# Kernel optimization log

Hardware: AMD Instinct MI355X
Metric: run time of the kernel (lower is better)

## Reference

```python
import jax, jax.numpy as jnp
import numpy as np

# DAttentionBaseline config (matches init_kwargs)
NH, HC, G = 8, 32, 4          # n_heads, n_head_channels, n_groups
ORF = 2.0                      # offset_range_factor
KK = 5                         # offset conv kernel (stage_idx=2)


def _conv1x1(x, w, b=None):
    # x: (B,C,H,W), w: (O,C)
    y = jnp.einsum('bchw,oc->bohw', x, w)
    return y if b is None else y + b[None, :, None, None]


def _ref_points(Hk, Wk, dtype):
    # replicates torch.meshgrid(..., indexing='xy') as in the source
    ly = jnp.linspace(0.5, Hk - 0.5, Hk, dtype=dtype)
    lx = jnp.linspace(0.5, Wk - 0.5, Wk, dtype=dtype)
    ry, rx = jnp.meshgrid(ly, lx, indexing='xy')  # shapes (Wk, Hk); Hk==Wk here
    return jnp.stack([ry / Hk * 2 - 1, rx / Wk * 2 - 1], axis=-1)  # (Hk,Wk,2)


def _grid_sample(img, grid):
    # bilinear, align_corners=True, zero padding. img:(N,C,Hi,Wi), grid:(N,Hg,Wg,2) in [-1,1] (x,y)
    N, C, Hi, Wi = img.shape
    gx = (grid[..., 0] + 1.0) * 0.5 * (Wi - 1)
    gy = (grid[..., 1] + 1.0) * 0.5 * (Hi - 1)
    x0 = jnp.floor(gx); y0 = jnp.floor(gy)
    x1 = x0 + 1.0;      y1 = y0 + 1.0
    wx1 = gx - x0; wx0 = 1.0 - wx1
    wy1 = gy - y0; wy0 = 1.0 - wy1
    nidx = jnp.arange(N)[:, None, None]

    def gather(yf, xf):
        valid = (xf >= 0) & (xf <= Wi - 1) & (yf >= 0) & (yf <= Hi - 1)
        xi = jnp.clip(xf, 0, Wi - 1).astype(jnp.int32)
        yi = jnp.clip(yf, 0, Hi - 1).astype(jnp.int32)
        vals = img[nidx, :, yi, xi]  # (N,Hg,Wg,C)
        return vals * valid[..., None].astype(img.dtype)

    out = (gather(y0, x0) * (wy0 * wx0)[..., None]
           + gather(y0, x1) * (wy0 * wx1)[..., None]
           + gather(y1, x0) * (wy1 * wx0)[..., None]
           + gather(y1, x1) * (wy1 * wx1)[..., None])
    return out.transpose(0, 3, 1, 2)  # (N,C,Hg,Wg)


def _forward(x, wq, bq, w_off_dw, b_off_dw, ln_g, ln_b, w_off_pj, wk, bk, wv, bv, wo, bo, rpe_table):
    B, C, H, W = x.shape
    GC = C // G            # group channels
    GH = NH // G           # group heads
    scale = HC ** -0.5

    q = _conv1x1(x, wq, bq)                                   # (B,C,H,W)
    q_off = q.reshape(B * G, GC, H, W)

    # conv_offset: depthwise conv -> LayerNorm over channels -> GELU -> 1x1 conv to 2
    off = jax.lax.conv_general_dilated(
        q_off, w_off_dw, (1, 1), [(KK // 2, KK // 2), (KK // 2, KK // 2)],
        feature_group_count=GC, dimension_numbers=('NCHW', 'OIHW', 'NCHW'))
    off = off + b_off_dw[None, :, None, None]
    mu = off.mean(axis=1, keepdims=True)
    var = off.var(axis=1, keepdims=True)
    off = (off - mu) * jax.lax.rsqrt(var + 1e-5)
    off = off * ln_g[None, :, None, None] + ln_b[None, :, None, None]
    off = jax.nn.gelu(off, approximate=False)
    offset = jnp.einsum('bchw,oc->bohw', off, w_off_pj)       # (B*G,2,Hk,Wk)

    Hk, Wk = offset.shape[2], offset.shape[3]
    ns = Hk * Wk
    rng = jnp.array([1.0 / Hk, 1.0 / Wk], dtype=x.dtype).reshape(1, 2, 1, 1)
    offset = jnp.tanh(offset) * rng * ORF                     # offset_range_factor > 0
    offset = offset.transpose(0, 2, 3, 1)                     # (B*G,Hk,Wk,2)

    ref = _ref_points(Hk, Wk, x.dtype)                        # (Hk,Wk,2)
    pos = offset + ref[None]                                  # (B*G,Hk,Wk,2), (y,x) order

    xs = _grid_sample(x.reshape(B * G, GC, H, W), pos[..., ::-1])  # (B*G,GC,Hk,Wk)
    xs = xs.reshape(B, C, 1, ns)

    k = _conv1x1(xs, wk, bk).reshape(B * NH, HC, ns)
    v = _conv1x1(xs, wv, bv).reshape(B * NH, HC, ns)
    qf = q.reshape(B * NH, HC, H * W)
    attn = jnp.einsum('bcm,bcn->bmn', qf, k) * scale          # (B*NH, HW, ns)

    # RPE via grid_sample on the (2H-1, 2W-1) bias table
    rpe = jnp.broadcast_to(rpe_table[None], (B,) + rpe_table.shape)
    rpe = rpe.reshape(B * G, GH, 2 * H - 1, 2 * W - 1)
    qg = _ref_points(H, W, x.dtype).reshape(H * W, 2)
    disp = (qg[None, :, None, :] - pos.reshape(B * G, ns, 2)[:, None, :, :]) * 0.5  # (B*G,HW,ns,2)
    bias = _grid_sample(rpe, disp[..., ::-1]).reshape(B * NH, H * W, ns)
    attn = attn + bias

    attn = jax.nn.softmax(attn, axis=2)
    out = jnp.einsum('bmn,bcn->bcm', attn, v).reshape(B, C, H, W)
    y = _conv1x1(out, wo, bo)
    return (y,
            pos.reshape(B, G, Hk, Wk, 2),
            jnp.broadcast_to(ref[None, None], (B, G, Hk, Wk, 2)))


def setup_inputs() -> dict:
    key = jax.random.key(0)
    ks = jax.random.split(key, 8)
    B, C, H, W = 4, 256, 32, 32
    GC = C // G
    s = 0.02

    def n(k, shape, sc=s):
        return jax.random.normal(k, shape, jnp.float32) * sc

    return {
        'x': jax.random.normal(ks[0], (B, C, H, W), jnp.float32),
        'wq': n(ks[1], (C, C)), 'bq': jnp.zeros((C,), jnp.float32),
        'w_off_dw': n(ks[2], (GC, 1, KK, KK)), 'b_off_dw': jnp.zeros((GC,), jnp.float32),
        'ln_g': jnp.ones((GC,), jnp.float32), 'ln_b': jnp.zeros((GC,), jnp.float32),
        'w_off_pj': n(ks[3], (2, GC)),
        'wk': n(ks[4], (C, C)), 'bk': jnp.zeros((C,), jnp.float32),
        'wv': n(ks[5], (C, C)), 'bv': jnp.zeros((C,), jnp.float32),
        'wo': n(ks[6], (C, C)), 'bo': jnp.zeros((C,), jnp.float32),
        'rpe_table': n(ks[7], (NH, 2 * H - 1, 2 * W - 1), 0.01),
    }


def reference(x, wq, bq, w_off_dw, b_off_dw, ln_g, ln_b, w_off_pj, wk, bk, wv, bv, wo, bo, rpe_table):
    return _forward(x, wq, bq, w_off_dw, b_off_dw, ln_g, ln_b, w_off_pj, wk, bk, wv, bv, wo, bo, rpe_table)
```

## Files before the change

kernel.cpp:

```cpp
#include <hip/hip_runtime.h>
#include <math.h>

#define CK __restrict__

constexpr int CH = 256;
constexpr int HW = 1024;

typedef __attribute__((ext_vector_type(8))) short short8;
typedef __attribute__((ext_vector_type(4))) float f32x4;

__device__ __forceinline__ ushort f2b(float x) {
    union { float f; unsigned int u; } a; a.f = x;
    unsigned int r = (a.u + 0x7FFFu + ((a.u >> 16) & 1u)) >> 16;
    return (ushort)r;
}
__device__ __forceinline__ short8 ld8(const ushort* p) { return *(const short8*)p; }
__device__ __forceinline__ float u2f(unsigned int u) {
    union { unsigned int u; float f; } a; a.u = u; return a.f;
}
__device__ __forceinline__ float b2f(ushort us) { return u2f((unsigned int)us << 16); }

__global__ __launch_bounds__(256) void prep(const float* CK w0, const float* CK w1,
                                            const float* CK w2, const float* CK w3,
                                            ushort* CK o0, ushort* CK o1,
                                            ushort* CK o2, ushort* CK o3,
                                            const float* CK x, ushort* CK xT,
                                            const float* CK rpe, unsigned int* CK rpetab) {
    const int bid = blockIdx.x, t = threadIdx.x;
    if (bid < 256) {
        const float* src; ushort* dst;
        switch (bid >> 6) {
            case 0: src = w0; dst = o0; break;
            case 1: src = w1; dst = o1; break;
            case 2: src = w2; dst = o2; break;
            default: src = w3; dst = o3; break;
        }
        const int i = (bid & 63) * 256 + t;
        float4 v = ((const float4*)src)[i];
        ushort4 r; r.x = f2b(v.x); r.y = f2b(v.y); r.z = f2b(v.z); r.w = f2b(v.w);
        ((ushort4*)dst)[i] = r;
    } else if (bid < 384) {
        const int b2 = bid - 256;
        const int c8 = b2 & 31, b = b2 >> 5;
        for (int nn = 0; nn < 4; nn++) {
            const int n = nn * 256 + t;
            union { ushort u[8]; short8 s; } pk;
#pragma unroll
            for (int j = 0; j < 8; j++) pk.u[j] = f2b(x[(b * 256 + c8 * 8 + j) * HW + n]);
            *(short8*)(xT + b * 262144 + n * 256 + c8 * 8) = pk.s;
        }
    } else {
        const int h = bid - 384;
        const float* rp = rpe + h * 3969;
        unsigned int* dst = rpetab + h * 4356;
        for (int i = t; i < 4356; i += 256) {
            int y = i / 67, x2 = i - y * 67;
            int yy = y - 1, xx = x2 - 1;
            bool vy = (yy >= 0) && (yy < 63) && (y < 65);
            float a  = (vy && xx >= 0 && xx < 63) ? rp[yy * 63 + xx] : 0.f;
            float bb = (vy && xx >= -1 && xx < 62) ? rp[yy * 63 + xx + 1] : 0.f;
            dst[i] = (unsigned int)f2b(a) | ((unsigned int)f2b(bb) << 16);
        }
    }
}

__global__ __launch_bounds__(256) void gemm_f32(const ushort* CK AT, const ushort* CK W,
                                                const float* CK bias, float* CK Y) {
    const int b = blockIdx.z;
    const int t = threadIdx.x, w = t >> 6, l = t & 63;
    const int lm = l & 15, qd = l >> 4;
    const int m0 = blockIdx.y * 16;
    const int np = blockIdx.x * 64 + w * 16;
    const ushort* A  = AT + b * 262144 + (np + lm) * 256;
    const ushort* Bm = W + (m0 + lm) * 256;
    f32x4 acc = {0.f, 0.f, 0.f, 0.f};
#pragma unroll
    for (int k0 = 0; k0 < 8; k0++) {
        const int ko = k0 * 32 + qd * 8;
        acc = __builtin_amdgcn_mfma_f32_16x16x32_bf16(ld8(A + ko), ld8(Bm + ko), acc, 0, 0, 0);
    }
    const float bs = bias[m0 + lm];
    float4 r;
    r.x = acc[0] + bs; r.y = acc[1] + bs; r.z = acc[2] + bs; r.w = acc[3] + bs;
    *(float4*)(Y + b * 262144 + (m0 + lm) * HW + np + qd * 4) = r;
}

__global__ __launch_bounds__(256) void gemm_kv(const ushort* CK AT,
                                               const ushort* CK Wk, const float* CK bk, ushort* CK kbt,
                                               const ushort* CK Wv, const float* CK bv, ushort* CK vbs) {
    const int b = blockIdx.z;
    const int t = threadIdx.x, w = t >> 6, l = t & 63;
    const int lm = l & 15, qd = l >> 4;
    const int m0 = blockIdx.y * 16;
    const int np = blockIdx.x * 64 + w * 16;
    const ushort* A  = AT + b * 262144 + (np + lm) * 256;
    const ushort* Kw = Wk + (m0 + lm) * 256;
    const ushort* Vw = Wv + (m0 + lm) * 256;
    f32x4 akT = {0.f, 0.f, 0.f, 0.f}, av = {0.f, 0.f, 0.f, 0.f};
#pragma unroll
    for (int k0 = 0; k0 < 8; k0++) {
        const int ko = k0 * 32 + qd * 8;
        short8 a = ld8(A + ko);
        akT = __builtin_amdgcn_mfma_f32_16x16x32_bf16(ld8(Kw + ko), a, akT, 0, 0, 0);
        av  = __builtin_amdgcn_mfma_f32_16x16x32_bf16(a, ld8(Vw + ko), av, 0, 0, 0);
    }
    {
        const int ch0 = m0 + qd * 4;
        const int pix = np + lm;
        const int bh = b * 8 + (ch0 >> 5);
        const int qdk = (ch0 & 31) >> 3, co4 = ch0 & 7;
        const int nc = pix >> 7, nbk = (pix >> 4) & 7, lmk = pix & 15;
        const float4 bks = *(const float4*)(bk + ch0);
        ushort4 r4;
        r4.x = f2b(akT[0] + bks.x); r4.y = f2b(akT[1] + bks.y);
        r4.z = f2b(akT[2] + bks.z); r4.w = f2b(akT[3] + bks.w);
        *(ushort4*)(kbt + ((bh * 8 + nc) * 512 + nbk * 64 + qdk * 16 + lmk) * 8 + co4) = r4;
    }
    {
        const int ch = m0 + lm;
        const int pix0 = np + qd * 4;
        const int bh = b * 8 + (ch >> 5);
        const int cb = (ch & 31) >> 4, lmv = ch & 15;
        const int nc = pix0 >> 7, kc = (pix0 >> 5) & 3;
        const int qdv = (pix0 >> 3) & 3, co0 = pix0 & 7;
        const float bs = bv[ch];
        ushort4 r4;
        r4.x = f2b(av[0] + bs); r4.y = f2b(av[1] + bs);
        r4.z = f2b(av[2] + bs); r4.w = f2b(av[3] + bs);
        *(ushort4*)(vbs + ((bh * 8 + nc) * 512 + (cb * 4 + kc) * 64 + qdv * 16 + lmv) * 8 + co0) = r4;
    }
}

__global__ __launch_bounds__(256) void dwconv(const float* CK q, const float* CK wdw,
                                              const float* CK bdw, float* CK off) {
    const int bx = blockIdx.x;
    const int ch = bx & 63;
    const float* qb = q + bx * HW;
    float w[25];
#pragma unroll
    for (int i = 0; i < 25; i++) w[i] = wdw[ch * 25 + i];
    const float bb = bdw[ch];
    const int t = threadIdx.x;
#pragma unroll
    for (int p = 0; p < 4; p++) {
        int hw = p * 256 + t;
        int ii = hw >> 5, jj = hw & 31;
        float s = bb;
#pragma unroll
        for (int ky = 0; ky < 5; ky++) {
            int y = ii + ky - 2;
            if (y < 0 || y > 31) continue;
#pragma unroll
            for (int kx = 0; kx < 5; kx++) {
                int x = jj + kx - 2;
                if (x < 0 || x > 31) continue;
                s += qb[y * 32 + x] * w[ky * 5 + kx];
            }
        }
        off[bx * HW + hw] = s;
    }
}

__global__ __launch_bounds__(256) void lnps(const float* CK off, const float* CK ln_g,
                                            const float* CK ln_b, const float* CK wpj,
                                            const float* CK x,
                                            float* CK out_pos, float* CK out_ref,
                                            float2* CK pos_sc, ushort* CK xsT) {
    const int bid = blockIdx.x, t = threadIdx.x;
    const int bg = bid >> 4;
    const int pix_l = t >> 2, qtr = t & 3;
    const int n = (bid & 15) * 64 + pix_l;
    const int gid = bg * 1024 + n;
    const float* ob = off + bg * 64 * HW + n;
    const int c0 = qtr * 16;
    float s1 = 0.f;
#pragma unroll
    for (int j = 0; j < 16; j++) s1 += ob[(c0 + j) * HW];
    s1 += __shfl_xor(s1, 1); s1 += __shfl_xor(s1, 2);
    const float mean = s1 * 0.015625f;
    float s2 = 0.f;
#pragma unroll
    for (int j = 0; j < 16; j++) { float d = ob[(c0 + j) * HW] - mean; s2 += d * d; }
    s2 += __shfl_xor(s2, 1); s2 += __shfl_xor(s2, 2);
    const float rs = rsqrtf(s2 * 0.015625f + 1e-5f);
    float p0 = 0.f, p1 = 0.f;
#pragma unroll
    for (int j = 0; j < 16; j++) {
        float vv = (ob[(c0 + j) * HW] - mean) * rs * ln_g[c0 + j] + ln_b[c0 + j];
        float gl = 0.5f * vv * (1.f + erff(vv * 0.70710678118654752f));
        p0 += gl * wpj[c0 + j];
        p1 += gl * wpj[64 + c0 + j];
    }
    p0 += __shfl_xor(p0, 1); p0 += __shfl_xor(p0, 2);
    p1 += __shfl_xor(p1, 1); p1 += __shfl_xor(p1, 2);
    const int ii = n >> 5, jj = n & 31;
    const float r0 = (jj + 0.5f) * 0.0625f - 1.f;
    const float r1 = (ii + 0.5f) * 0.0625f - 1.f;
    const float pos0 = tanhf(p0) * 0.0625f + r0;
    const float pos1 = tanhf(p1) * 0.0625f + r1;
    if (qtr == 0) {
        out_pos[gid * 2] = pos0; out_pos[gid * 2 + 1] = pos1;
        out_ref[gid * 2] = r0;   out_ref[gid * 2 + 1] = r1;
        pos_sc[gid].x = pos0 * 15.5f; pos_sc[gid].y = pos1 * 15.5f;
    }
    const float gx = (pos1 + 1.f) * 15.5f, gy = (pos0 + 1.f) * 15.5f;
    const float x0f = floorf(gx), y0f = floorf(gy);
    const float wx1 = gx - x0f, wx0 = 1.f - wx1, wy1 = gy - y0f, wy0 = 1.f - wy1;
    const bool vx0 = (x0f >= 0.f) && (x0f <= 31.f);
    const bool vx1 = (x0f >= -1.f) && (x0f <= 30.f);
    const bool vy0 = (y0f >= 0.f) && (y0f <= 31.f);
    const bool vy1 = (y0f >= -1.f) && (y0f <= 30.f);
    const int xi0 = (int)fminf(fmaxf(x0f, 0.f), 31.f);
    const int xi1 = (int)fminf(fmaxf(x0f + 1.f, 0.f), 31.f);
    const int yi0 = (int)fminf(fmaxf(y0f, 0.f), 31.f);
    const int yi1 = (int)fminf(fmaxf(y0f + 1.f, 0.f), 31.f);
    const float w00 = (vy0 && vx0) ? wy0 * wx0 : 0.f;
    const float w01 = (vy0 && vx1) ? wy0 * wx1 : 0.f;
    const float w10 = (vy1 && vx0) ? wy1 * wx0 : 0.f;
    const float w11 = (vy1 && vx1) ? wy1 * wx1 : 0.f;
    const int o00 = yi0 * 32 + xi0, o01 = yi0 * 32 + xi1;
    const int o10 = yi1 * 32 + xi0, o11 = yi1 * 32 + xi1;
    const int b = bg >> 2, g = bg & 3;
    const float* xb = x + bg * 64 * HW;
    ushort* xo = xsT + b * 262144 + n * 256 + g * 64 + c0;
#pragma unroll
    for (int j4 = 0; j4 < 4; j4++) {
        ushort4 r4;
        float vals[4];
#pragma unroll
        for (int j = 0; j < 4; j++) {
            const float* p = xb + (c0 + j4 * 4 + j) * HW;
            vals[j] = w00 * p[o00] + w01 * p[o01] + w10 * p[o10] + w11 * p[o11];
        }
        r4.x = f2b(vals[0]); r4.y = f2b(vals[1]); r4.z = f2b(vals[2]); r4.w = f2b(vals[3]);
        *(ushort4*)(xo + j4 * 4) = r4;
    }
}

__global__ __launch_bounds__(256, 4) void attn_part(const float* CK q, const ushort* CK kbt,
                                                    const ushort* CK vbs, const float2* CK pos_sc,
                                                    const unsigned int* CK rpetab,
                                                    ushort* CK partO, float2* CK mlbuf) {
    __shared__ __align__(16) unsigned int rpe_pr[4356];
    __shared__ __align__(16) ushort Pl[4][2176];
    const int bh = blockIdx.y, half = blockIdx.z;
    const int b = bh >> 3, nh = bh & 7, bg = bh >> 1;
    const int t = threadIdx.x;
    const int w = t >> 6, l = t & 63;
    const int lm = l & 15, qd = l >> 4;

    {
        const uint4* src4 = (const uint4*)(rpetab + nh * 4356);
        uint4* dst4 = (uint4*)rpe_pr;
        for (int i = t; i < 1089; i += 256) dst4[i] = src4[i];
    }
    __syncthreads();

    const int m = blockIdx.x * 64 + w * 16 + lm;
    short8 qf;
    {
        union { ushort u[8]; short8 s; } pk;
        const float* qb = q + (b * 256 + nh * 32) * HW + m;
#pragma unroll
        for (int j = 0; j < 8; j++) pk.u[j] = f2b(qb[(qd * 8 + j) * HW]);
        qf = pk.s;
    }
    const float qg0 = ((m & 31) + 0.5f) * 0.0625f - 1.f;
    const float qg1 = ((m >> 5) + 0.5f) * 0.0625f - 1.f;
    const float ax = 31.f + 15.5f * qg1;
    const float ay = 31.f + 15.5f * qg0;

    f32x4 oacc0 = {0.f, 0.f, 0.f, 0.f}, oacc1 = {0.f, 0.f, 0.f, 0.f};
    float rmax = -3e38f, rsum = 0.f;
    ushort* PlW = Pl[w];
    const float2* pbase = pos_sc + bg * 1024;

    for (int nc = half * 4; nc < half * 4 + 4; nc++) {
        const ushort* kg = kbt + (bh * 8 + nc) * 4096;
        const ushort* vg = vbs + (bh * 8 + nc) * 4096;

        f32x4 sT[8];
#pragma unroll
        for (int nb = 0; nb < 8; nb++) {
            sT[nb] = __builtin_amdgcn_mfma_f32_16x16x32_bf16(ld8(kg + (nb * 64 + l) * 8), qf,
                        (f32x4){0.f, 0.f, 0.f, 0.f}, 0, 0, 0);
        }

        float cmax = -3e38f;
#pragma unroll
        for (int nb = 0; nb < 8; nb++) {
            const float4* pp = (const float4*)(pbase + nc * 128 + nb * 16 + qd * 4);
            const float4 pa = pp[0], pb_ = pp[1];
            const float psx[4] = {pa.x, pa.z, pb_.x, pb_.z};
            const float psy[4] = {pa.y, pa.w, pb_.y, pb_.w};
#pragma unroll
            for (int r = 0; r < 4; r++) {
                const float gx = ax - psy[r];
                const float gy = ay - psx[r];
                const float x0f = floorf(gx), y0f = floorf(gy);
                const float wx1 = gx - x0f, wy1 = gy - y0f;
                const int idx = (int)y0f * 67 + (int)x0f + 68;
                const unsigned int pr0 = rpe_pr[idx];
                const unsigned int pr1 = rpe_pr[idx + 67];
                const float t00 = u2f(pr0 << 16), t01 = u2f(pr0 & 0xFFFF0000u);
                const float t10 = u2f(pr1 << 16), t11 = u2f(pr1 & 0xFFFF0000u);
                const float u0 = t00 + wx1 * (t01 - t00);
                const float u1 = t10 + wx1 * (t11 - t10);
                const float bias = u0 + wy1 * (u1 - u0);
                sT[nb][r] = sT[nb][r] * 0.17677669529663687f + bias;
                cmax = fmaxf(cmax, sT[nb][r]);
            }
        }
        cmax = fmaxf(cmax, __shfl_xor(cmax, 16));
        cmax = fmaxf(cmax, __shfl_xor(cmax, 32));
        const float newmax = fmaxf(rmax, cmax);
        const float alpha = __expf(rmax - newmax);
        rmax = newmax;

        float csum = 0.f;
#pragma unroll
        for (int nb = 0; nb < 8; nb++) {
            float e0 = __expf(sT[nb][0] - rmax);
            float e1 = __expf(sT[nb][1] - rmax);
            float e2 = __expf(sT[nb][2] - rmax);
            float e3 = __expf(sT[nb][3] - rmax);
            csum += (e0 + e1) + (e2 + e3);
            uint2 pk;
            pk.x = (unsigned int)f2b(e0) | ((unsigned int)f2b(e1) << 16);
            pk.y = (unsigned int)f2b(e2) | ((unsigned int)f2b(e3) << 16);
            *(uint2*)(PlW + nb * 272 + l * 4) = pk;
        }
        csum += __shfl_xor(csum, 16);
        csum += __shfl_xor(csum, 32);
        rsum = rsum * alpha + csum;
        oacc0 *= alpha;
        oacc1 *= alpha;

#pragma unroll
        for (int kc = 0; kc < 4; kc++) {
            const ushort* pb2 = PlW + (kc * 2 + (qd >> 1)) * 272 + (qd & 1) * 128 + lm * 4;
            union { uint2 u[2]; short8 s; } pfu;
            pfu.u[0] = *(const uint2*)pb2;
            pfu.u[1] = *(const uint2*)(pb2 + 64);
            oacc0 = __builtin_amdgcn_mfma_f32_16x16x32_bf16(ld8(vg + (kc * 64 + l) * 8), pfu.s, oacc0, 0, 0, 0);
            oacc1 = __builtin_amdgcn_mfma_f32_16x16x32_bf16(ld8(vg + ((4 + kc) * 64 + l) * 8), pfu.s, oacc1, 0, 0, 0);
        }
    }

    ushort* po = partO + (((half * 32 + bh) * 1024 + m) * 32) + qd * 4;
    ushort4 r04, r14;
    r04.x = f2b(oacc0[0]); r04.y = f2b(oacc0[1]); r04.z = f2b(oacc0[2]); r04.w = f2b(oacc0[3]);
    r14.x = f2b(oacc1[0]); r14.y = f2b(oacc1[1]); r14.z = f2b(oacc1[2]); r14.w = f2b(oacc1[3]);
    *(ushort4*)po = r04;
    *(ushort4*)(po + 16) = r14;
    if (qd == 0) {
        float2 ml; ml.x = rmax; ml.y = rsum;
        mlbuf[(half * 32 + bh) * 1024 + m] = ml;
    }
}

__global__ __launch_bounds__(256) void attn_comb(const ushort* CK partO, const float2* CK mlbuf,
                                                 ushort* CK aoT) {
    const int gid = blockIdx.x * 256 + threadIdx.x;
    const int bh = gid >> 10, m = gid & 1023;
    const int b = bh >> 3, nh = bh & 7;
    const float2 ml0 = mlbuf[bh * 1024 + m];
    const float2 ml1 = mlbuf[(32 + bh) * 1024 + m];
    const float M = fmaxf(ml0.x, ml1.x);
    const float e0 = __expf(ml0.x - M), e1 = __expf(ml1.x - M);
    const float inv = 1.f / (ml0.y * e0 + ml1.y * e1);
    const float w0 = e0 * inv, w1 = e1 * inv;
    const ushort* p0 = partO + (bh * 1024 + m) * 32;
    const ushort* p1 = partO + ((32 + bh) * 1024 + m) * 32;
    ushort* ob = aoT + b * 262144 + m * 256 + nh * 32;
#pragma unroll
    for (int h = 0; h < 2; h++) {
        union { ushort u[8]; short8 s; } a, c, o;
        a.s = ld8(p0 + h * 8 + (h >> 1) * 0);
        a.s = ld8(p0 + h * 16);
        c.s = ld8(p1 + h * 16);
#pragma unroll
        for (int j = 0; j < 8; j++) o.u[j] = f2b(b2f(a.u[j]) * w0 + b2f(c.u[j]) * w1);
        *(short8*)(ob + h * 16) = o.s;
        union { ushort u[8]; short8 s; } a2, c2, o2;
        a2.s = ld8(p0 + h * 16 + 8);
        c2.s = ld8(p1 + h * 16 + 8);
#pragma unroll
        for (int j = 0; j < 8; j++) o2.u[j] = f2b(b2f(a2.u[j]) * w0 + b2f(c2.u[j]) * w1);
        *(short8*)(ob + h * 16 + 8) = o2.s;
    }
}

extern "C" void kernel_launch(void* const* d_in, const int* in_sizes, int n_in,
                              void* d_out, int out_size, void* d_ws, size_t ws_size,
                              hipStream_t stream) {
    (void)in_sizes; (void)n_in; (void)out_size; (void)ws_size;
    const float* x   = (const float*)d_in[0];
    const float* wq  = (const float*)d_in[1];
    const float* bq  = (const float*)d_in[2];
    const float* wdw = (const float*)d_in[3];
    const float* bdw = (const float*)d_in[4];
    const float* lng = (const float*)d_in[5];
    const float* lnb = (const float*)d_in[6];
    const float* wpj = (const float*)d_in[7];
    const float* wk  = (const float*)d_in[8];
    const float* bk  = (const float*)d_in[9];
    const float* wv  = (const float*)d_in[10];
    const float* bv  = (const float*)d_in[11];
    const float* wo  = (const float*)d_in[12];
    const float* bo  = (const float*)d_in[13];
    const float* rpe = (const float*)d_in[14];
    float* outp = (float*)d_out;
    char* base = (char*)d_ws;
    const size_t MB = 1 << 20;

    float*  q_ws   = (float*)(base);
    float*  off_ws = (float*)(base + 4 * MB);
    ushort* partO  = (ushort*)(base + 4 * MB);
    float2* pos_sc = (float2*)(base + 8 * MB);
    ushort* xT     = (ushort*)(base + 8 * MB + 131072);
    float2* mlbuf  = (float2*)(base + 8 * MB + 131072);
    ushort* xsT    = (ushort*)(base + 10 * MB + 131072);
    ushort* kbt    = (ushort*)(base + 12 * MB + 131072);
    ushort* vbs    = (ushort*)(base + 14 * MB + 131072);
    ushort* aoT    = (ushort*)(base + 16 * MB + 131072);
    ushort* wqb    = (ushort*)(base + 18 * MB + 131072);
    ushort* wkb    = (ushort*)(base + 18 * MB + 262144);
    ushort* wvb    = (ushort*)(base + 18 * MB + 393216);
    ushort* wob    = (ushort*)(base + 18 * MB + 524288);
    unsigned int* rpetab = (unsigned int*)(base + 18 * MB + 655360);

    prep<<<392, 256, 0, stream>>>(wq, wk, wv, wo, wqb, wkb, wvb, wob, x, xT, rpe, rpetab);
    gemm_f32<<<dim3(16, 16, 4), 256, 0, stream>>>(xT, wqb, bq, q_ws);
    dwconv<<<1024, 256, 0, stream>>>(q_ws, wdw, bdw, off_ws);
    lnps<<<256, 256, 0, stream>>>(off_ws, lng, lnb, wpj, x,
                                  outp + (1 << 20), outp + (1 << 20) + 32768, pos_sc, xsT);
    gemm_kv<<<dim3(16, 16, 4), 256, 0, stream>>>(xsT, wkb, bk, kbt, wvb, bv, vbs);
    attn_part<<<dim3(16, 32, 2), 256, 0, stream>>>(q_ws, kbt, vbs, pos_sc, rpetab, partO, mlbuf);
    attn_comb<<<128, 256, 0, stream>>>(partO, mlbuf, aoT);
    gemm_f32<<<dim3(16, 16, 4), 256, 0, stream>>>(aoT, wob, bo, outp);
}
```

Measured before the change: 202.8 us.

## Retile GEMMs to 32x32 per wave, store q in bf16, split attention four ways

The GEMMs now have each wave compute a 2x2 block of 16x16 MFMA tiles, so A and B fragments are reused and the grid is a quarter of its former size. The Q projection output is written as bf16, which halves its traffic into dwconv and attention and removes the conversion inside attention. Attention splits keys into four partitions instead of two, processes keys in smaller chunks with a smaller LDS buffer and a higher occupancy hint, and the combine kernel merges four partials. LayerNorm caches its loaded values in registers, and the workspace layout is reorganised. Rounding q to bf16 earlier slightly changes the numerics of the offset path, and the finer online-softmax chunks add more rescaling steps.

```diff
diff --git a/kernel.cpp b/kernel.cpp
--- a/kernel.cpp
+++ b/kernel.cpp
@@ -64,25 +64,74 @@
     }
 }
 
-__global__ __launch_bounds__(256) void gemm_f32(const ushort* CK AT, const ushort* CK W,
-                                                const float* CK bias, float* CK Y) {
+__global__ __launch_bounds__(256) void gemm_q(const ushort* CK AT, const ushort* CK W,
+                                              const float* CK bias, ushort* CK Y) {
     const int b = blockIdx.z;
     const int t = threadIdx.x, w = t >> 6, l = t & 63;
     const int lm = l & 15, qd = l >> 4;
-    const int m0 = blockIdx.y * 16;
-    const int np = blockIdx.x * 64 + w * 16;
-    const ushort* A  = AT + b * 262144 + (np + lm) * 256;
-    const ushort* Bm = W + (m0 + lm) * 256;
-    f32x4 acc = {0.f, 0.f, 0.f, 0.f};
+    const int m0 = blockIdx.y * 64 + (w & 1) * 32;
+    const int n0 = blockIdx.x * 64 + (w >> 1) * 32;
+    const ushort* A = AT + b * 262144 + n0 * 256;
+    const ushort* Bm = W + m0 * 256;
+    f32x4 acc[2][2] = {};
 #pragma unroll
     for (int k0 = 0; k0 < 8; k0++) {
         const int ko = k0 * 32 + qd * 8;
-        acc = __builtin_amdgcn_mfma_f32_16x16x32_bf16(ld8(A + ko), ld8(Bm + ko), acc, 0, 0, 0);
-    }
-    const float bs = bias[m0 + lm];
-    float4 r;
-    r.x = acc[0] + bs; r.y = acc[1] + bs; r.z = acc[2] + bs; r.w = acc[3] + bs;
-    *(float4*)(Y + b * 262144 + (m0 + lm) * HW + np + qd * 4) = r;
+        short8 a0 = ld8(A + lm * 256 + ko);
+        short8 a1 = ld8(A + (16 + lm) * 256 + ko);
+        short8 b0 = ld8(Bm + lm * 256 + ko);
+        short8 b1 = ld8(Bm + (16 + lm) * 256 + ko);
+        acc[0][0] = __builtin_amdgcn_mfma_f32_16x16x32_bf16(a0, b0, acc[0][0], 0, 0, 0);
+        acc[0][1] = __builtin_amdgcn_mfma_f32_16x16x32_bf16(a0, b1, acc[0][1], 0, 0, 0);
+        acc[1][0] = __builtin_amdgcn_mfma_f32_16x16x32_bf16(a1, b0, acc[1][0], 0, 0, 0);
+        acc[1][1] = __builtin_amdgcn_mfma_f32_16x16x32_bf16(a1, b1, acc[1][1], 0, 0, 0);
+    }
+#pragma unroll
+    for (int in = 0; in < 2; in++)
+#pragma unroll
+        for (int im = 0; im < 2; im++) {
+            const int m = m0 + im * 16 + lm;
+            const float bs = bias[m];
+            ushort4 r;
+            r.x = f2b(acc[in][im][0] + bs); r.y = f2b(acc[in][im][1] + bs);
+            r.z = f2b(acc[in][im][2] + bs); r.w = f2b(acc[in][im][3] + bs);
+            *(ushort4*)(Y + b * 262144 + m * HW + n0 + in * 16 + qd * 4) = r;
+        }
+}
+
+__global__ __launch_bounds__(256) void gemm_o(const ushort* CK AT, const ushort* CK W,
+                                              const float* CK bias, float* CK Y) {
+    const int b = blockIdx.z;
+    const int t = threadIdx.x, w = t >> 6, l = t & 63;
+    const int lm = l & 15, qd = l >> 4;
+    const int m0 = blockIdx.y * 64 + (w & 1) * 32;
+    const int n0 = blockIdx.x * 64 + (w >> 1) * 32;
+    const ushort* A = AT + b * 262144 + n0 * 256;
+    const ushort* Bm = W + m0 * 256;
+    f32x4 acc[2][2] = {};
+#pragma unroll
+    for (int k0 = 0; k0 < 8; k0++) {
+        const int ko = k0 * 32 + qd * 8;
+        short8 a0 = ld8(A + lm * 256 + ko);
+        short8 a1 = ld8(A + (16 + lm) * 256 + ko);
+        short8 b0 = ld8(Bm + lm * 256 + ko);
+        short8 b1 = ld8(Bm + (16 + lm) * 256 + ko);
+        acc[0][0] = __builtin_amdgcn_mfma_f32_16x16x32_bf16(a0, b0, acc[0][0], 0, 0, 0);
+        acc[0][1] = __builtin_amdgcn_mfma_f32_16x16x32_bf16(a0, b1, acc[0][1], 0, 0, 0);
+        acc[1][0] = __builtin_amdgcn_mfma_f32_16x16x32_bf16(a1, b0, acc[1][0], 0, 0, 0);
+        acc[1][1] = __builtin_amdgcn_mfma_f32_16x16x32_bf16(a1, b1, acc[1][1], 0, 0, 0);
+    }
+#pragma unroll
+    for (int in = 0; in < 2; in++)
+#pragma unroll
+        for (int im = 0; im < 2; im++) {
+            const int m = m0 + im * 16 + lm;
+            const float bs = bias[m];
+            float4 r;
+            r.x = acc[in][im][0] + bs; r.y = acc[in][im][1] + bs;
+            r.z = acc[in][im][2] + bs; r.w = acc[in][im][3] + bs;
+            *(float4*)(Y + b * 262144 + m * HW + n0 + in * 16 + qd * 4) = r;
+        }
 }
 
 __global__ __launch_bounds__(256) void gemm_kv(const ushort* CK AT,
@@ -91,51 +140,69 @@
     const int b = blockIdx.z;
     const int t = threadIdx.x, w = t >> 6, l = t & 63;
     const int lm = l & 15, qd = l >> 4;
-    const int m0 = blockIdx.y * 16;
-    const int np = blockIdx.x * 64 + w * 16;
-    const ushort* A  = AT + b * 262144 + (np + lm) * 256;
-    const ushort* Kw = Wk + (m0 + lm) * 256;
-    const ushort* Vw = Wv + (m0 + lm) * 256;
-    f32x4 akT = {0.f, 0.f, 0.f, 0.f}, av = {0.f, 0.f, 0.f, 0.f};
+    const int m0 = blockIdx.y * 64 + (w & 1) * 32;
+    const int n0 = blockIdx.x * 64 + (w >> 1) * 32;
+    const ushort* A = AT + b * 262144 + n0 * 256;
+    const ushort* Bk = Wk + m0 * 256;
+    const ushort* Bv = Wv + m0 * 256;
+    f32x4 akT[2][2] = {}, av[2][2] = {};
 #pragma unroll
     for (int k0 = 0; k0 < 8; k0++) {
         const int ko = k0 * 32 + qd * 8;
-        short8 a = ld8(A + ko);
-        akT = __builtin_amdgcn_mfma_f32_16x16x32_bf16(ld8(Kw + ko), a, akT, 0, 0, 0);
-        av  = __builtin_amdgcn_mfma_f32_16x16x32_bf16(a, ld8(Vw + ko), av, 0, 0, 0);
-    }
-    {
-        const int ch0 = m0 + qd * 4;
-        const int pix = np + lm;
-        const int bh = b * 8 + (ch0 >> 5);
-        const int qdk = (ch0 & 31) >> 3, co4 = ch0 & 7;
-        const int nc = pix >> 7, nbk = (pix >> 4) & 7, lmk = pix & 15;
-        const float4 bks = *(const float4*)(bk + ch0);
-        ushort4 r4;
-        r4.x = f2b(akT[0] + bks.x); r4.y = f2b(akT[1] + bks.y);
-        r4.z = f2b(akT[2] + bks.z); r4.w = f2b(akT[3] + bks.w);
-        *(ushort4*)(kbt + ((bh * 8 + nc) * 512 + nbk * 64 + qdk * 16 + lmk) * 8 + co4) = r4;
-    }
-    {
-        const int ch = m0 + lm;
-        const int pix0 = np + qd * 4;
-        const int bh = b * 8 + (ch >> 5);
-        const int cb = (ch & 31) >> 4, lmv = ch & 15;
-        const int nc = pix0 >> 7, kc = (pix0 >> 5) & 3;
-        const int qdv = (pix0 >> 3) & 3, co0 = pix0 & 7;
-        const float bs = bv[ch];
-        ushort4 r4;
-        r4.x = f2b(av[0] + bs); r4.y = f2b(av[1] + bs);
-        r4.z = f2b(av[2] + bs); r4.w = f2b(av[3] + bs);
-        *(ushort4*)(vbs + ((bh * 8 + nc) * 512 + (cb * 4 + kc) * 64 + qdv * 16 + lmv) * 8 + co0) = r4;
-    }
-}
-
-__global__ __launch_bounds__(256) void dwconv(const float* CK q, const float* CK wdw,
+        short8 a0 = ld8(A + lm * 256 + ko);
+        short8 a1 = ld8(A + (16 + lm) * 256 + ko);
+        short8 k0f = ld8(Bk + lm * 256 + ko);
+        short8 k1f = ld8(Bk + (16 + lm) * 256 + ko);
+        short8 v0f = ld8(Bv + lm * 256 + ko);
+        short8 v1f = ld8(Bv + (16 + lm) * 256 + ko);
+        akT[0][0] = __builtin_amdgcn_mfma_f32_16x16x32_bf16(k0f, a0, akT[0][0], 0, 0, 0);
+        akT[0][1] = __builtin_amdgcn_mfma_f32_16x16x32_bf16(k0f, a1, akT[0][1], 0, 0, 0);
+        akT[1][0] = __builtin_amdgcn_mfma_f32_16x16x32_bf16(k1f, a0, akT[1][0], 0, 0, 0);
+        akT[1][1] = __builtin_amdgcn_mfma_f32_16x16x32_bf16(k1f, a1, akT[1][1], 0, 0, 0);
+        av[0][0] = __builtin_amdgcn_mfma_f32_16x16x32_bf16(a0, v0f, av[0][0], 0, 0, 0);
+        av[0][1] = __builtin_amdgcn_mfma_f32_16x16x32_bf16(a0, v1f, av[0][1], 0, 0, 0);
+        av[1][0] = __builtin_amdgcn_mfma_f32_16x16x32_bf16(a1, v0f, av[1][0], 0, 0, 0);
+        av[1][1] = __builtin_amdgcn_mfma_f32_16x16x32_bf16(a1, v1f, av[1][1], 0, 0, 0);
+    }
+#pragma unroll
+    for (int im = 0; im < 2; im++)
+#pragma unroll
+        for (int in = 0; in < 2; in++) {
+            {
+                const int c0 = m0 + im * 16 + qd * 4;
+                const int n  = n0 + in * 16 + lm;
+                const int bh = b * 8 + (c0 >> 5);
+                const int qdk = (c0 & 31) >> 3, co4 = c0 & 7;
+                const int nc = n >> 7, nbk = (n >> 4) & 7, lmk = n & 15;
+                const float4 bks = *(const float4*)(bk + c0);
+                ushort4 r4;
+                r4.x = f2b(akT[im][in][0] + bks.x);
+                r4.y = f2b(akT[im][in][1] + bks.y);
+                r4.z = f2b(akT[im][in][2] + bks.z);
+                r4.w = f2b(akT[im][in][3] + bks.w);
+                *(ushort4*)(kbt + ((bh * 8 + nc) * 512 + nbk * 64 + qdk * 16 + lmk) * 8 + co4) = r4;
+            }
+            {
+                const int c = m0 + im * 16 + lm;
+                const int bh = b * 8 + (c >> 5);
+                const float bs = bv[c];
+                const int cb = (c & 31) >> 4, lmv = c & 15;
+                const int nbase = n0 + in * 16 + qd * 4;
+                const int nc = nbase >> 7, kc = (nbase >> 5) & 3;
+                const int qdv = (nbase >> 3) & 3, co0 = nbase & 7;
+                ushort4 r4;
+                r4.x = f2b(av[in][im][0] + bs); r4.y = f2b(av[in][im][1] + bs);
+                r4.z = f2b(av[in][im][2] + bs); r4.w = f2b(av[in][im][3] + bs);
+                *(ushort4*)(vbs + ((bh * 8 + nc) * 512 + (cb * 4 + kc) * 64 + qdv * 16 + lmv) * 8 + co0) = r4;
+            }
+        }
+}
+
+__global__ __launch_bounds__(256) void dwconv(const ushort* CK q, const float* CK wdw,
                                               const float* CK bdw, float* CK off) {
     const int bx = blockIdx.x;
     const int ch = bx & 63;
-    const float* qb = q + bx * HW;
+    const ushort* qb = q + bx * HW;
     float w[25];
 #pragma unroll
     for (int i = 0; i < 25; i++) w[i] = wdw[ch * 25 + i];
@@ -154,7 +221,7 @@
             for (int kx = 0; kx < 5; kx++) {
                 int x = jj + kx - 2;
                 if (x < 0 || x > 31) continue;
-                s += qb[y * 32 + x] * w[ky * 5 + kx];
+                s += b2f(qb[y * 32 + x]) * w[ky * 5 + kx];
             }
         }
         off[bx * HW + hw] = s;
@@ -173,20 +240,21 @@
     const int gid = bg * 1024 + n;
     const float* ob = off + bg * 64 * HW + n;
     const int c0 = qtr * 16;
+    float v[16];
     float s1 = 0.f;
 #pragma unroll
-    for (int j = 0; j < 16; j++) s1 += ob[(c0 + j) * HW];
+    for (int j = 0; j < 16; j++) { v[j] = ob[(c0 + j) * HW]; s1 += v[j]; }
     s1 += __shfl_xor(s1, 1); s1 += __shfl_xor(s1, 2);
     const float mean = s1 * 0.015625f;
     float s2 = 0.f;
 #pragma unroll
-    for (int j = 0; j < 16; j++) { float d = ob[(c0 + j) * HW] - mean; s2 += d * d; }
+    for (int j = 0; j < 16; j++) { float d = v[j] - mean; s2 += d * d; }
     s2 += __shfl_xor(s2, 1); s2 += __shfl_xor(s2, 2);
     const float rs = rsqrtf(s2 * 0.015625f + 1e-5f);
     float p0 = 0.f, p1 = 0.f;
 #pragma unroll
     for (int j = 0; j < 16; j++) {
-        float vv = (ob[(c0 + j) * HW] - mean) * rs * ln_g[c0 + j] + ln_b[c0 + j];
+        float vv = (v[j] - mean) * rs * ln_g[c0 + j] + ln_b[c0 + j];
         float gl = 0.5f * vv * (1.f + erff(vv * 0.70710678118654752f));
         p0 += gl * wpj[c0 + j];
         p1 += gl * wpj[64 + c0 + j];
@@ -237,13 +305,13 @@
     }
 }
 
-__global__ __launch_bounds__(256, 4) void attn_part(const float* CK q, const ushort* CK kbt,
+__global__ __launch_bounds__(256, 7) void attn_part(const ushort* CK q, const ushort* CK kbt,
                                                     const ushort* CK vbs, const float2* CK pos_sc,
                                                     const unsigned int* CK rpetab,
                                                     ushort* CK partO, float2* CK mlbuf) {
     __shared__ __align__(16) unsigned int rpe_pr[4356];
-    __shared__ __align__(16) ushort Pl[4][2176];
-    const int bh = blockIdx.y, half = blockIdx.z;
+    __shared__ __align__(16) ushort Pl[4][544];
+    const int bh = blockIdx.y, quarter = blockIdx.z;
     const int b = bh >> 3, nh = bh & 7, bg = bh >> 1;
     const int t = threadIdx.x;
     const int w = t >> 6, l = t & 63;
@@ -260,9 +328,9 @@
     short8 qf;
     {
         union { ushort u[8]; short8 s; } pk;
-        const float* qb = q + (b * 256 + nh * 32) * HW + m;
-#pragma unroll
-        for (int j = 0; j < 8; j++) pk.u[j] = f2b(qb[(qd * 8 + j) * HW]);
+        const ushort* qb = q + (b * 256 + nh * 32) * HW + m;
+#pragma unroll
+        for (int j = 0; j < 8; j++) pk.u[j] = qb[(qd * 8 + j) * HW];
         qf = pk.s;
     }
     const float qg0 = ((m & 31) + 0.5f) * 0.0625f - 1.f;
@@ -275,79 +343,77 @@
     ushort* PlW = Pl[w];
     const float2* pbase = pos_sc + bg * 1024;
 
-    for (int nc = half * 4; nc < half * 4 + 4; nc++) {
+    for (int nc = quarter * 2; nc < quarter * 2 + 2; nc++) {
         const ushort* kg = kbt + (bh * 8 + nc) * 4096;
         const ushort* vg = vbs + (bh * 8 + nc) * 4096;
 
-        f32x4 sT[8];
-#pragma unroll
-        for (int nb = 0; nb < 8; nb++) {
-            sT[nb] = __builtin_amdgcn_mfma_f32_16x16x32_bf16(ld8(kg + (nb * 64 + l) * 8), qf,
-                        (f32x4){0.f, 0.f, 0.f, 0.f}, 0, 0, 0);
-        }
-
-        float cmax = -3e38f;
-#pragma unroll
-        for (int nb = 0; nb < 8; nb++) {
-            const float4* pp = (const float4*)(pbase + nc * 128 + nb * 16 + qd * 4);
-            const float4 pa = pp[0], pb_ = pp[1];
-            const float psx[4] = {pa.x, pa.z, pb_.x, pb_.z};
-            const float psy[4] = {pa.y, pa.w, pb_.y, pb_.w};
-#pragma unroll
-            for (int r = 0; r < 4; r++) {
-                const float gx = ax - psy[r];
-                const float gy = ay - psx[r];
-                const float x0f = floorf(gx), y0f = floorf(gy);
-                const float wx1 = gx - x0f, wy1 = gy - y0f;
-                const int idx = (int)y0f * 67 + (int)x0f + 68;
-                const unsigned int pr0 = rpe_pr[idx];
-                const unsigned int pr1 = rpe_pr[idx + 67];
-                const float t00 = u2f(pr0 << 16), t01 = u2f(pr0 & 0xFFFF0000u);
-                const float t10 = u2f(pr1 << 16), t11 = u2f(pr1 & 0xFFFF0000u);
-                const float u0 = t00 + wx1 * (t01 - t00);
-                const float u1 = t10 + wx1 * (t11 - t10);
-                const float bias = u0 + wy1 * (u1 - u0);
-                sT[nb][r] = sT[nb][r] * 0.17677669529663687f + bias;
-                cmax = fmaxf(cmax, sT[nb][r]);
+#pragma unroll
+        for (int nb2 = 0; nb2 < 4; nb2++) {
+            f32x4 sT[2];
+#pragma unroll
+            for (int s = 0; s < 2; s++) {
+                const int nb = nb2 * 2 + s;
+                sT[s] = __builtin_amdgcn_mfma_f32_16x16x32_bf16(
+                            ld8(kg + (nb * 64 + l) * 8), qf,
+                            (f32x4){0.f, 0.f, 0.f, 0.f}, 0, 0, 0);
             }
-        }
-        cmax = fmaxf(cmax, __shfl_xor(cmax, 16));
-        cmax = fmaxf(cmax, __shfl_xor(cmax, 32));
-        const float newmax = fmaxf(rmax, cmax);
-        const float alpha = __expf(rmax - newmax);
-        rmax = newmax;
-
-        float csum = 0.f;
-#pragma unroll
-        for (int nb = 0; nb < 8; nb++) {
-            float e0 = __expf(sT[nb][0] - rmax);
-            float e1 = __expf(sT[nb][1] - rmax);
-            float e2 = __expf(sT[nb][2] - rmax);
-            float e3 = __expf(sT[nb][3] - rmax);
-            csum += (e0 + e1) + (e2 + e3);
-            uint2 pk;
-            pk.x = (unsigned int)f2b(e0) | ((unsigned int)f2b(e1) << 16);
-            pk.y = (unsigned int)f2b(e2) | ((unsigned int)f2b(e3) << 16);
-            *(uint2*)(PlW + nb * 272 + l * 4) = pk;
-        }
-        csum += __shfl_xor(csum, 16);
-        csum += __shfl_xor(csum, 32);
-        rsum = rsum * alpha + csum;
-        oacc0 *= alpha;
-        oacc1 *= alpha;
-
-#pragma unroll
-        for (int kc = 0; kc < 4; kc++) {
-            const ushort* pb2 = PlW + (kc * 2 + (qd >> 1)) * 272 + (qd & 1) * 128 + lm * 4;
+            float cmax = -3e38f;
+#pragma unroll
+            for (int s = 0; s < 2; s++) {
+                const float4* pp = (const float4*)(pbase + nc * 128 + (nb2 * 2 + s) * 16 + qd * 4);
+                const float4 pa = pp[0], pb_ = pp[1];
+                const float psx[4] = {pa.x, pa.z, pb_.x, pb_.z};
+                const float psy[4] = {pa.y, pa.w, pb_.y, pb_.w};
+#pragma unroll
+                for (int r = 0; r < 4; r++) {
+                    const float gx = ax - psy[r];
+                    const float gy = ay - psx[r];
+                    const float x0f = floorf(gx), y0f = floorf(gy);
+                    const float wx1 = gx - x0f, wy1 = gy - y0f;
+                    const int idx = (int)y0f * 67 + (int)x0f + 68;
+                    const unsigned int pr0 = rpe_pr[idx];
+                    const unsigned int pr1 = rpe_pr[idx + 67];
+                    const float t00 = u2f(pr0 << 16), t01 = u2f(pr0 & 0xFFFF0000u);
+                    const float t10 = u2f(pr1 << 16), t11 = u2f(pr1 & 0xFFFF0000u);
+                    const float u0 = t00 + wx1 * (t01 - t00);
+                    const float u1 = t10 + wx1 * (t11 - t10);
+                    sT[s][r] = sT[s][r] * 0.17677669529663687f + (u0 + wy1 * (u1 - u0));
+                    cmax = fmaxf(cmax, sT[s][r]);
+                }
+            }
+            cmax = fmaxf(cmax, __shfl_xor(cmax, 16));
+            cmax = fmaxf(cmax, __shfl_xor(cmax, 32));
+            const float newmax = fmaxf(rmax, cmax);
+            const float alpha = __expf(rmax - newmax);
+            rmax = newmax;
+            float csum = 0.f;
+#pragma unroll
+            for (int s = 0; s < 2; s++) {
+                float e0 = __expf(sT[s][0] - rmax);
+                float e1 = __expf(sT[s][1] - rmax);
+                float e2 = __expf(sT[s][2] - rmax);
+                float e3 = __expf(sT[s][3] - rmax);
+                csum += (e0 + e1) + (e2 + e3);
+                uint2 pk;
+                pk.x = (unsigned int)f2b(e0) | ((unsigned int)f2b(e1) << 16);
+                pk.y = (unsigned int)f2b(e2) | ((unsigned int)f2b(e3) << 16);
+                *(uint2*)(PlW + s * 272 + l * 4) = pk;
+            }
+            csum += __shfl_xor(csum, 16);
+            csum += __shfl_xor(csum, 32);
+            rsum = rsum * alpha + csum;
+            oacc0 *= alpha;
+            oacc1 *= alpha;
+            const ushort* pb2 = PlW + (qd >> 1) * 272 + (qd & 1) * 128 + lm * 4;
             union { uint2 u[2]; short8 s; } pfu;
             pfu.u[0] = *(const uint2*)pb2;
             pfu.u[1] = *(const uint2*)(pb2 + 64);
-            oacc0 = __builtin_amdgcn_mfma_f32_16x16x32_bf16(ld8(vg + (kc * 64 + l) * 8), pfu.s, oacc0, 0, 0, 0);
-            oacc1 = __builtin_amdgcn_mfma_f32_16x16x32_bf16(ld8(vg + ((4 + kc) * 64 + l) * 8), pfu.s, oacc1, 0, 0, 0);
-        }
-    }
-
-    ushort* po = partO + (((half * 32 + bh) * 1024 + m) * 32) + qd * 4;
+            oacc0 = __builtin_amdgcn_mfma_f32_16x16x32_bf16(ld8(vg + (nb2 * 64 + l) * 8), pfu.s, oacc0, 0, 0, 0);
+            oacc1 = __builtin_amdgcn_mfma_f32_16x16x32_bf16(ld8(vg + ((4 + nb2) * 64 + l) * 8), pfu.s, oacc1, 0, 0, 0);
+        }
+    }
+
+    ushort* po = partO + (((quarter * 32 + bh) * 1024 + m) * 32) + qd * 4;
     ushort4 r04, r14;
     r04.x = f2b(oacc0[0]); r04.y = f2b(oacc0[1]); r04.z = f2b(oacc0[2]); r04.w = f2b(oacc0[3]);
     r14.x = f2b(oacc1[0]); r14.y = f2b(oacc1[1]); r14.z = f2b(oacc1[2]); r14.w = f2b(oacc1[3]);
@@ -355,39 +421,40 @@
     *(ushort4*)(po + 16) = r14;
     if (qd == 0) {
         float2 ml; ml.x = rmax; ml.y = rsum;
-        mlbuf[(half * 32 + bh) * 1024 + m] = ml;
-    }
-}
-
-__global__ __launch_bounds__(256) void attn_comb(const ushort* CK partO, const float2* CK mlbuf,
+        mlbuf[(quarter * 32 + bh) * 1024 + m] = ml;
+    }
+}
+
+__global__ __launch_bounds__(128) void attn_comb(const ushort* CK partO, const float2* CK mlbuf,
                                                  ushort* CK aoT) {
-    const int gid = blockIdx.x * 256 + threadIdx.x;
+    const int gid = blockIdx.x * 128 + threadIdx.x;
     const int bh = gid >> 10, m = gid & 1023;
     const int b = bh >> 3, nh = bh & 7;
-    const float2 ml0 = mlbuf[bh * 1024 + m];
-    const float2 ml1 = mlbuf[(32 + bh) * 1024 + m];
-    const float M = fmaxf(ml0.x, ml1.x);
-    const float e0 = __expf(ml0.x - M), e1 = __expf(ml1.x - M);
-    const float inv = 1.f / (ml0.y * e0 + ml1.y * e1);
-    const float w0 = e0 * inv, w1 = e1 * inv;
-    const ushort* p0 = partO + (bh * 1024 + m) * 32;
-    const ushort* p1 = partO + ((32 + bh) * 1024 + m) * 32;
+    float2 ml[4];
+    float M = -3e38f;
+#pragma unroll
+    for (int i = 0; i < 4; i++) { ml[i] = mlbuf[(i * 32 + bh) * 1024 + m]; M = fmaxf(M, ml[i].x); }
+    float e[4], denom = 0.f;
+#pragma unroll
+    for (int i = 0; i < 4; i++) { e[i] = __expf(ml[i].x - M); denom += ml[i].y * e[i]; }
+    const float inv = 1.f / denom;
+#pragma unroll
+    for (int i = 0; i < 4; i++) e[i] *= inv;
     ushort* ob = aoT + b * 262144 + m * 256 + nh * 32;
 #pragma unroll
-    for (int h = 0; h < 2; h++) {
-        union { ushort u[8]; short8 s; } a, c, o;
-        a.s = ld8(p0 + h * 8 + (h >> 1) * 0);
-        a.s = ld8(p0 + h * 16);
-        c.s = ld8(p1 + h * 16);
-#pragma unroll
-        for (int j = 0; j < 8; j++) o.u[j] = f2b(b2f(a.u[j]) * w0 + b2f(c.u[j]) * w1);
-        *(short8*)(ob + h * 16) = o.s;
-        union { ushort u[8]; short8 s; } a2, c2, o2;
-        a2.s = ld8(p0 + h * 16 + 8);
-        c2.s = ld8(p1 + h * 16 + 8);
-#pragma unroll
-        for (int j = 0; j < 8; j++) o2.u[j] = f2b(b2f(a2.u[j]) * w0 + b2f(c2.u[j]) * w1);
-        *(short8*)(ob + h * 16 + 8) = o2.s;
+    for (int g8 = 0; g8 < 4; g8++) {
+        float acc[8] = {};
+#pragma unroll
+        for (int i = 0; i < 4; i++) {
+            union { ushort u[8]; short8 s; } pv;
+            pv.s = ld8(partO + ((i * 32 + bh) * 1024 + m) * 32 + g8 * 8);
+#pragma unroll
+            for (int j = 0; j < 8; j++) acc[j] += b2f(pv.u[j]) * e[i];
+        }
+        union { ushort u[8]; short8 s; } o;
+#pragma unroll
+        for (int j = 0; j < 8; j++) o.u[j] = f2b(acc[j]);
+        *(short8*)(ob + g8 * 8) = o.s;
     }
 }
 
@@ -414,29 +481,29 @@
     char* base = (char*)d_ws;
     const size_t MB = 1 << 20;
 
-    float*  q_ws   = (float*)(base);
-    float*  off_ws = (float*)(base + 4 * MB);
-    ushort* partO  = (ushort*)(base + 4 * MB);
-    float2* pos_sc = (float2*)(base + 8 * MB);
-    ushort* xT     = (ushort*)(base + 8 * MB + 131072);
-    float2* mlbuf  = (float2*)(base + 8 * MB + 131072);
-    ushort* xsT    = (ushort*)(base + 10 * MB + 131072);
-    ushort* kbt    = (ushort*)(base + 12 * MB + 131072);
-    ushort* vbs    = (ushort*)(base + 14 * MB + 131072);
-    ushort* aoT    = (ushort*)(base + 16 * MB + 131072);
-    ushort* wqb    = (ushort*)(base + 18 * MB + 131072);
-    ushort* wkb    = (ushort*)(base + 18 * MB + 262144);
-    ushort* wvb    = (ushort*)(base + 18 * MB + 393216);
-    ushort* wob    = (ushort*)(base + 18 * MB + 524288);
-    unsigned int* rpetab = (unsigned int*)(base + 18 * MB + 655360);
+    ushort* q_b    = (ushort*)(base);
+    ushort* kbt    = (ushort*)(base + 2 * MB);
+    ushort* vbs    = (ushort*)(base + 4 * MB);
+    float*  off_ws = (float*)(base + 6 * MB);
+    ushort* xT     = (ushort*)(base + 10 * MB);
+    ushort* xsT    = (ushort*)(base + 12 * MB);
+    ushort* partO  = (ushort*)(base + 6 * MB);
+    float2* mlbuf  = (float2*)(base + 14 * MB);
+    ushort* aoT    = (ushort*)(base + 15 * MB);
+    ushort* wqb    = (ushort*)(base + 17 * MB);
+    ushort* wkb    = (ushort*)(base + 17 * MB + 131072);
+    ushort* wvb    = (ushort*)(base + 17 * MB + 262144);
+    ushort* wob    = (ushort*)(base + 17 * MB + 393216);
+    float2* pos_sc = (float2*)(base + 17 * MB + 524288);
+    unsigned int* rpetab = (unsigned int*)(base + 17 * MB + 655360);
 
     prep<<<392, 256, 0, stream>>>(wq, wk, wv, wo, wqb, wkb, wvb, wob, x, xT, rpe, rpetab);
-    gemm_f32<<<dim3(16, 16, 4), 256, 0, stream>>>(xT, wqb, bq, q_ws);
-    dwconv<<<1024, 256, 0, stream>>>(q_ws, wdw, bdw, off_ws);
+    gemm_q<<<dim3(16, 4, 4), 256, 0, stream>>>(xT, wqb, bq, q_b);
+    dwconv<<<1024, 256, 0, stream>>>(q_b, wdw, bdw, off_ws);
     lnps<<<256, 256, 0, stream>>>(off_ws, lng, lnb, wpj, x,
                                   outp + (1 << 20), outp + (1 << 20) + 32768, pos_sc, xsT);
-    gemm_kv<<<dim3(16, 16, 4), 256, 0, stream>>>(xsT, wkb, bk, kbt, wvb, bv, vbs);
-    attn_part<<<dim3(16, 32, 2), 256, 0, stream>>>(q_ws, kbt, vbs, pos_sc, rpetab, partO, mlbuf);
-    attn_comb<<<128, 256, 0, stream>>>(partO, mlbuf, aoT);
-    gemm_f32<<<dim3(16, 16, 4), 256, 0, stream>>>(aoT, wob, bo, outp);
-}
+    gemm_kv<<<dim3(16, 4, 4), 256, 0, stream>>>(xsT, wkb, bk, kbt, wvb, bv, vbs);
+    attn_part<<<dim3(16, 32, 4), 256, 0, stream>>>(q_b, kbt, vbs, pos_sc, rpetab, partO, mlbuf);
+    attn_comb<<<256, 128, 0, stream>>>(partO, mlbuf, aoT);
+    gemm_o<<<dim3(16, 4, 4), 256, 0, stream>>>(aoT, wob, bo, outp);
+}
```

Measured after the change: 188.8 us. -6.9%, faster.
